# Kernel optimization log

Hardware: AMD Instinct MI355X
Metric: run time of the kernel (lower is better)

The kernel has to match this reference:

```python
import jax, jax.numpy as jnp
import numpy as np


def setup_inputs() -> dict:
    key = jax.random.key(0)
    ks = jax.random.split(key, 6)
    B, Lq, Lk, D = 8, 2048, 2048, 128
    return {
        "query": jax.random.normal(ks[0], (B, Lq, D), dtype=jnp.float32),
        "x": jax.random.normal(ks[1], (B, Lk, D), dtype=jnp.float32),
        "valid": jax.random.randint(ks[2], (B, Lq, Lk), 0, 2, dtype=jnp.int32),
        "Wq": jax.random.normal(ks[3], (D, D), dtype=jnp.float32) * 0.05,
        "Wk": jax.random.normal(ks[4], (D, D), dtype=jnp.float32) * 0.05,
        "Wv": jax.random.normal(ks[5], (D, D), dtype=jnp.float32) * 0.05,
    }


def reference(query, x, valid, Wq, Wk, Wv):
    # bias-free linear projections; torch Linear weight is [out, in] -> y = x @ W.T
    q = jnp.einsum("bqd,ad->bqa", query, Wq)   # [B, Lq, D]
    k = jnp.einsum("bkd,ad->bka", x, Wk)        # [B, Lk, D]
    v = jnp.einsum("bkd,ad->bka", x, Wv)        # [B, Lk, D]
    # scores (no scale arg passed in this config)
    att = jnp.einsum("bqd,bkd->bqk", q, k)      # [B, Lq, Lk]
    # max-subtraction BEFORE masking (matches original op order)
    att = att - jnp.max(att, axis=-1, keepdims=True)
    att = jnp.where(valid <= 0, -jnp.inf, att)
    att_w = jax.nn.softmax(att, axis=-1)
    # rows with all entries masked produce NaN -> fill with 0
    att_w = jnp.where(jnp.isnan(att_w), jnp.zeros_like(att_w), att_w)
    result = jnp.einsum("bqk,bkd->bqd", att_w, v)
    return (result, att_w)
```

## Files before the change

kernel.cpp:

```cpp
#include <hip/hip_runtime.h>
#include <float.h>
#include <math.h>


#define BB 8
#define LQ 2048
#define LK 2048
#define DD 128
#define NROWS (BB*LQ)
#define KS 4

typedef __attribute__((ext_vector_type(8))) _Float16 half8;
typedef __attribute__((ext_vector_type(4))) float f32x4;

#define QH_OFF  (0u)
#define QL_OFF  (1u*NROWS*DD*2u)
#define KH_OFF  (2u*NROWS*DD*2u)
#define KL_OFF  (3u*NROWS*DD*2u)
#define VTH_OFF (4u*NROWS*DD*2u)
#define VTL_OFF (5u*NROWS*DD*2u)
#define BM_OFF  (6u*NROWS*DD*2u)
#define MZ_OFF  (BM_OFF + (unsigned)NROWS*(LK/8))

__device__ __forceinline__ f32x4 mfma16(half8 a, half8 b, f32x4 c) {
  return __builtin_amdgcn_mfma_f32_16x16x32_f16(a, b, c, 0, 0, 0);
}

__global__ __launch_bounds__(256, 3) void proj_kernel(
    const float* __restrict__ query, const float* __restrict__ x,
    const float* __restrict__ Wq, const float* __restrict__ Wk,
    const float* __restrict__ Wv, unsigned char* __restrict__ wsb)
{
  __shared__ float SB[8704];
  const int which = blockIdx.y;
  const float* __restrict__ src = (which == 0) ? query : x;
  const float* __restrict__ W   = (which == 0) ? Wq : (which == 1 ? Wk : Wv);
  const int t = threadIdx.x, l = t & 63, wv = t >> 6;
  const int lr = l & 15, lg = l >> 4;
  const int r0 = blockIdx.x * 64;

#pragma unroll
  for (int j = 0; j < 8; ++j) {
    const int flat = j * 1024 + t * 4;
    const int row = flat >> 7, col = flat & 127;
    *(float4*)&SB[row * 132 + col] = *(const float4*)&src[(size_t)(r0 + row) * DD + col];
  }
  __syncthreads();

  half8 ah[4], al[4];
#pragma unroll
  for (int dc = 0; dc < 4; ++dc) {
    const int base = (wv * 16 + lr) * 132 + dc * 32 + lg * 8;
    float4 f0 = *(const float4*)&SB[base];
    float4 f1 = *(const float4*)&SB[base + 4];
    float f[8] = {f0.x, f0.y, f0.z, f0.w, f1.x, f1.y, f1.z, f1.w};
#pragma unroll
    for (int e = 0; e < 8; ++e) {
      _Float16 h = (_Float16)f[e];
      ah[dc][e] = h;
      al[dc][e] = (_Float16)(f[e] - (float)h);
    }
  }
  __syncthreads();

  f32x4 acc[8];
#pragma unroll
  for (int a = 0; a < 8; ++a) acc[a] = (f32x4){0.f, 0.f, 0.f, 0.f};

#pragma unroll
  for (int dc = 0; dc < 4; ++dc) {
#pragma unroll
    for (int a = 0; a < 8; ++a) {
      const float* p = W + (size_t)(a * 16 + lr) * DD + dc * 32 + lg * 8;
      float4 f0 = *(const float4*)p;
      float4 f1 = *(const float4*)(p + 4);
      float f[8] = {f0.x, f0.y, f0.z, f0.w, f1.x, f1.y, f1.z, f1.w};
      half8 bh, bl;
#pragma unroll
      for (int e = 0; e < 8; ++e) {
        _Float16 h = (_Float16)f[e];
        bh[e] = h;
        bl[e] = (_Float16)(f[e] - (float)h);
      }
      acc[a] = mfma16(ah[dc], bh, acc[a]);
      acc[a] = mfma16(al[dc], bh, acc[a]);
      acc[a] = mfma16(ah[dc], bl, acc[a]);
    }
  }

  if (which < 2) {
    _Float16* Oh = (_Float16*)(wsb + (which == 0 ? QH_OFF : KH_OFF));
    _Float16* Ol = (_Float16*)(wsb + (which == 0 ? QL_OFF : KL_OFF));
#pragma unroll
    for (int a = 0; a < 8; ++a)
#pragma unroll
      for (int i = 0; i < 4; ++i) {
        const int ro = r0 + wv * 16 + lg * 4 + i;
        const int co = a * 16 + lr;
        float v = acc[a][i];
        _Float16 h = (_Float16)v;
        Oh[(size_t)ro * DD + co] = h;
        Ol[(size_t)ro * DD + co] = (_Float16)(v - (float)h);
      }
  } else {
    _Float16* TH = (_Float16*)SB;
    _Float16* TL = TH + 8704;
#pragma unroll
    for (int a = 0; a < 8; ++a)
#pragma unroll
      for (int i = 0; i < 4; ++i) {
        const int rl = wv * 16 + lg * 4 + i;
        const int co = a * 16 + lr;
        float v = acc[a][i];
        _Float16 h = (_Float16)v;
        TH[co * 68 + rl] = h;
        TL[co * 68 + rl] = (_Float16)(v - (float)h);
      }
    __syncthreads();
    _Float16* Vh = (_Float16*)(wsb + VTH_OFF);
    _Float16* Vl = (_Float16*)(wsb + VTL_OFF);
    const int b = r0 >> 11, kloc = r0 & 2047;
    const int d = t >> 1, hh = t & 1;
    const size_t gb = ((size_t)(b * DD + d)) * LK + kloc + hh * 32;
#pragma unroll
    for (int j = 0; j < 8; ++j) {
      *(ushort4*)(Vh + gb + j * 4) = *(const ushort4*)&TH[d * 68 + hh * 32 + j * 4];
      *(ushort4*)(Vl + gb + j * 4) = *(const ushort4*)&TL[d * 68 + hh * 32 + j * 4];
    }
  }
}

__global__ __launch_bounds__(256) void maskpack_kernel(
    const int* __restrict__ valid, unsigned long long* __restrict__ bm)
{
  const int t = threadIdx.x, l = t & 63, wv = t >> 6;
  const size_t base = (size_t)blockIdx.x * 32768 + (size_t)wv * 8192;
  for (int it = 0; it < 32; ++it) {
    int v0 = valid[base + (size_t)(it * 4 + 0) * 64 + l];
    int v1 = valid[base + (size_t)(it * 4 + 1) * 64 + l];
    int v2 = valid[base + (size_t)(it * 4 + 2) * 64 + l];
    int v3 = valid[base + (size_t)(it * 4 + 3) * 64 + l];
    unsigned long long m0 = __ballot(v0 > 0);
    unsigned long long m1 = __ballot(v1 > 0);
    unsigned long long m2 = __ballot(v2 > 0);
    unsigned long long m3 = __ballot(v3 > 0);
    if (l == 0) {
      bm[(base >> 6) + it * 4 + 0] = m0;
      bm[(base >> 6) + it * 4 + 1] = m1;
      bm[(base >> 6) + it * 4 + 2] = m2;
      bm[(base >> 6) + it * 4 + 3] = m3;
    }
  }
}

__global__ __launch_bounds__(256, 4) void scores_kernel(
    const unsigned char* __restrict__ wsb, float* __restrict__ att)
{
  __shared__ _Float16 KHs[64 * 128];
  __shared__ _Float16 KLs[64 * 128];
  const int t = threadIdx.x, l = t & 63, wv = t >> 6;
  const int lr = l & 15, lg = l >> 4;
  const int qb = blockIdx.x, b = blockIdx.y, ks = blockIdx.z;
  const int rowg = b * LQ + qb * 64;
  const int kbase = ks * 512;
  const _Float16* QH = (const _Float16*)(wsb + QH_OFF);
  const _Float16* QL = (const _Float16*)(wsb + QL_OFF);
  const _Float16* KH = (const _Float16*)(wsb + KH_OFF);
  const _Float16* KL = (const _Float16*)(wsb + KL_OFF);
  const unsigned* bm32 = (const unsigned*)(wsb + BM_OFF);
  float* M = (float*)(wsb + MZ_OFF);
  float* Z = M + KS * NROWS;

  half8 qh[4], ql[4];
#pragma unroll
  for (int dc = 0; dc < 4; ++dc) {
    const size_t idx = ((size_t)(rowg + wv * 16 + lr)) * DD + dc * 32 + lg * 8;
    qh[dc] = *(const half8*)(QH + idx);
    ql[dc] = *(const half8*)(QL + idx);
  }

  half8 rh[4], rl[4];
  auto issue_stage = [&](int kt) {
#pragma unroll
    for (int j = 0; j < 4; ++j) {
      const int flat = j * 2048 + t * 8;
      const int row = flat >> 7, col = flat & 127;
      const size_t g = ((size_t)(b * LK + kbase + kt * 64 + row)) * DD + col;
      rh[j] = *(const half8*)(KH + g);
      rl[j] = *(const half8*)(KL + g);
    }
  };
  auto write_stage = [&]() {
#pragma unroll
    for (int j = 0; j < 4; ++j) {
      const int flat = j * 2048 + t * 8;
      const int row = flat >> 7, c8 = (flat >> 3) & 15;
      const int c8s = (c8 & 8) | ((c8 ^ row) & 7);
      *(half8*)&KHs[row * 128 + c8s * 8] = rh[j];
      *(half8*)&KLs[row * 128 + c8s * 8] = rl[j];
    }
  };

  issue_stage(0);
  write_stage();

  float m_run[4], z_run[4];
#pragma unroll
  for (int i = 0; i < 4; ++i) { m_run[i] = -FLT_MAX; z_run[i] = 0.f; }

  for (int kt = 0; kt < 8; ++kt) {
    const int k0 = kbase + kt * 64;
    if (kt < 7) issue_stage(kt + 1);
    unsigned mw0[4], mw1[4];
#pragma unroll
    for (int i = 0; i < 4; ++i) {
      uint2 u = *(const uint2*)(bm32 + ((size_t)(rowg + wv * 16 + lg * 4 + i)) * 64 + (k0 >> 5));
      mw0[i] = u.x; mw1[i] = u.y;
    }
    __syncthreads();

    f32x4 acc[4];
#pragma unroll
    for (int kg = 0; kg < 4; ++kg) acc[kg] = (f32x4){0.f, 0.f, 0.f, 0.f};
#pragma unroll
    for (int kg = 0; kg < 4; ++kg)
#pragma unroll
      for (int dc = 0; dc < 4; ++dc) {
        const int c8 = dc * 4 + lg;
        const int c8s = (c8 & 8) | ((c8 ^ lr) & 7);
        half8 bh = *(const half8*)&KHs[(kg * 16 + lr) * 128 + c8s * 8];
        half8 bl = *(const half8*)&KLs[(kg * 16 + lr) * 128 + c8s * 8];
        acc[kg] = mfma16(qh[dc], bh, acc[kg]);
        acc[kg] = mfma16(ql[dc], bh, acc[kg]);
        acc[kg] = mfma16(qh[dc], bl, acc[kg]);
      }

#pragma unroll
    for (int i = 0; i < 4; ++i) {
      float sv[4];
      float* ap = att + ((size_t)(rowg + wv * 16 + lg * 4 + i)) * LK + k0 + lr;
#pragma unroll
      for (int kg = 0; kg < 4; ++kg) {
        unsigned w = (kg < 2) ? mw0[i] : mw1[i];
        int bit = (w >> (((kg & 1) * 16) + lr)) & 1;
        float v = bit ? acc[kg][i] : -INFINITY;
        sv[kg] = v;
        ap[kg * 16] = v;
      }
      float tm = fmaxf(fmaxf(sv[0], sv[1]), fmaxf(sv[2], sv[3]));
#pragma unroll
      for (int o = 1; o < 16; o <<= 1) tm = fmaxf(tm, __shfl_xor(tm, o));
      const float mo = m_run[i], mn = fmaxf(mo, tm);
      float za = __expf(sv[0] - mn) + __expf(sv[1] - mn) +
                 __expf(sv[2] - mn) + __expf(sv[3] - mn);
      z_run[i] = z_run[i] * __expf(mo - mn) + za;
      m_run[i] = mn;
    }
    __syncthreads();
    if (kt < 7) write_stage();
  }

#pragma unroll
  for (int i = 0; i < 4; ++i) {
    float z = z_run[i];
#pragma unroll
    for (int o = 1; o < 16; o <<= 1) z += __shfl_xor(z, o);
    if (lr == 0) {
      const size_t row = (size_t)(rowg + wv * 16 + lg * 4 + i);
      M[(size_t)ks * NROWS + row] = m_run[i];
      Z[(size_t)ks * NROWS + row] = z;
    }
  }
}

__global__ __launch_bounds__(256, 4) void pv_kernel(
    const unsigned char* __restrict__ wsb, float* __restrict__ att,
    float* __restrict__ res)
{
  __shared__ _Float16 VHs[128 * 64];
  __shared__ _Float16 Wt[64 * 64];
  const int t = threadIdx.x, l = t & 63, wv = t >> 6;
  const int lr = l & 15, lg = l >> 4;
  const int qb = blockIdx.x, b = blockIdx.y, kp = blockIdx.z;
  const int rowg = b * LQ + qb * 64;
  const int kbase = kp * 512;
  const _Float16* VTH = (const _Float16*)(wsb + VTH_OFF);
  const float* M = (const float*)(wsb + MZ_OFF);
  const float* Z = M + KS * NROWS;

  const int srow = t >> 2, scb = (t & 3) * 16;
  float mg, zi;
  {
    const size_t row = (size_t)(rowg + srow);
    float m0 = M[row], m1 = M[NROWS + row], m2 = M[2 * NROWS + row], m3 = M[3 * NROWS + row];
    mg = fmaxf(fmaxf(m0, m1), fmaxf(m2, m3));
    float z = Z[row] * __expf(m0 - mg) + Z[NROWS + row] * __expf(m1 - mg) +
              Z[2 * NROWS + row] * __expf(m2 - mg) + Z[3 * NROWS + row] * __expf(m3 - mg);
    zi = (z > 0.f) ? 1.f / z : 0.f;
  }

  half8 vhr[4];
  float4 sr[4];
  auto issue_V = [&](int kt) {
#pragma unroll
    for (int j = 0; j < 4; ++j) {
      const int flat = j * 2048 + t * 8;
      const int d = flat >> 6, kk = flat & 63;
      vhr[j] = *(const half8*)(VTH + ((size_t)(b * DD + d)) * LK + kbase + kt * 64 + kk);
    }
  };
  auto issue_S = [&](int kt) {
    const size_t rb = (size_t)(rowg + srow) * LK + kbase + kt * 64 + scb;
#pragma unroll
    for (int j = 0; j < 4; ++j) sr[j] = *(const float4*)&att[rb + j * 4];
  };
  auto w_stage = [&](int kt) {
    const size_t rb = (size_t)(rowg + srow) * LK + kbase + kt * 64 + scb;
    float wf[16];
#pragma unroll
    for (int j = 0; j < 4; ++j) {
      float4 w4;
      w4.x = __expf(sr[j].x - mg) * zi;
      w4.y = __expf(sr[j].y - mg) * zi;
      w4.z = __expf(sr[j].z - mg) * zi;
      w4.w = __expf(sr[j].w - mg) * zi;
      *(float4*)&att[rb + j * 4] = w4;
      wf[j * 4 + 0] = w4.x; wf[j * 4 + 1] = w4.y;
      wf[j * 4 + 2] = w4.z; wf[j * 4 + 3] = w4.w;
    }
    half8 h0, h1;
#pragma unroll
    for (int e = 0; e < 8; ++e) { h0[e] = (_Float16)wf[e]; h1[e] = (_Float16)wf[8 + e]; }
    const int g0 = (t & 3) * 2;
    *(half8*)&Wt[srow * 64 + (((g0)     ^ srow) & 7) * 8] = h0;
    *(half8*)&Wt[srow * 64 + (((g0 + 1) ^ srow) & 7) * 8] = h1;
#pragma unroll
    for (int j = 0; j < 4; ++j) {
      const int flat = j * 2048 + t * 8;
      const int d = flat >> 6, c8 = (flat >> 3) & 7;
      *(half8*)&VHs[d * 64 + ((c8 ^ d) & 7) * 8] = vhr[j];
    }
  };

  f32x4 oacc[8];
#pragma unroll
  for (int df = 0; df < 8; ++df) oacc[df] = (f32x4){0.f, 0.f, 0.f, 0.f};

  issue_V(0); issue_S(0);
  w_stage(0);
  __syncthreads();

  for (int kt = 0; kt < 8; ++kt) {
    if (kt < 7) { issue_V(kt + 1); issue_S(kt + 1); }

#pragma unroll
    for (int kc = 0; kc < 2; ++kc) {
      const int c8 = kc * 4 + lg;
      half8 wfr = *(const half8*)&Wt[(wv * 16 + lr) * 64 + ((c8 ^ (lr & 7)) & 7) * 8];
#pragma unroll
      for (int df = 0; df < 8; ++df) {
        half8 vh = *(const half8*)&VHs[(df * 16 + lr) * 64 + ((c8 ^ (lr & 7)) & 7) * 8];
        oacc[df] = mfma16(wfr, vh, oacc[df]);
      }
    }
    __syncthreads();
    if (kt < 7) {
      w_stage(kt + 1);
      __syncthreads();
    }
  }

#pragma unroll
  for (int df = 0; df < 8; ++df)
#pragma unroll
    for (int i = 0; i < 4; ++i)
      atomicAdd(&res[((size_t)(rowg + wv * 16 + lg * 4 + i)) * DD + df * 16 + lr],
                oacc[df][i]);
}

extern "C" void kernel_launch(void* const* d_in, const int* in_sizes, int n_in,
                              void* d_out, int out_size, void* d_ws, size_t ws_size,
                              hipStream_t stream)
{
  (void)in_sizes; (void)n_in; (void)out_size; (void)ws_size;
  const float* query = (const float*)d_in[0];
  const float* x     = (const float*)d_in[1];
  const int*   valid = (const int*)d_in[2];
  const float* Wq    = (const float*)d_in[3];
  const float* Wk    = (const float*)d_in[4];
  const float* Wv    = (const float*)d_in[5];

  float* out = (float*)d_out;
  float* res = out;
  float* att = out + (size_t)NROWS * DD;
  unsigned char* wsb = (unsigned char*)d_ws;

  hipMemsetAsync(res, 0, (size_t)NROWS * DD * sizeof(float), stream);
  proj_kernel<<<dim3(NROWS / 64, 3), 256, 0, stream>>>(query, x, Wq, Wk, Wv, wsb);
  maskpack_kernel<<<dim3(1024), 256, 0, stream>>>(
      valid, (unsigned long long*)(wsb + BM_OFF));
  scores_kernel<<<dim3(LQ / 64, BB, KS), 256, 0, stream>>>(wsb, att);
  pv_kernel<<<dim3(LQ / 64, BB, KS), 256, 0, stream>>>(wsb, att, res);
}
```

Before: 416.7 us.

## Fuse scores and PV into one two-pass kernel, drop K/V low-precision splits

Replaces the separate scores and PV kernels with one fused kernel per 32-query block. The first pass computes row max and sum; the second recomputes QK^T, writes normalized weights directly and accumulates P·V in LDS. This removes the att write/read round trip, the split-K atomics and the memset. K and V are now stored only as single fp16 (no low-part correction), which cuts projection stores and MFMA work but lowers precision. Recomputing QK doubles the score MFMAs, and the grid is smaller (512 blocks), which may reduce occupancy.

After: 365.5 us. -12.3%, faster.

```diff
diff --git a/kernel.cpp b/kernel.cpp
--- a/kernel.cpp
+++ b/kernel.cpp
@@ -8,19 +8,16 @@
 #define LK 2048
 #define DD 128
 #define NROWS (BB*LQ)
-#define KS 4
+#define QB 32
 
 typedef __attribute__((ext_vector_type(8))) _Float16 half8;
 typedef __attribute__((ext_vector_type(4))) float f32x4;
 
 #define QH_OFF  (0u)
-#define QL_OFF  (1u*NROWS*DD*2u)
-#define KH_OFF  (2u*NROWS*DD*2u)
-#define KL_OFF  (3u*NROWS*DD*2u)
-#define VTH_OFF (4u*NROWS*DD*2u)
-#define VTL_OFF (5u*NROWS*DD*2u)
-#define BM_OFF  (6u*NROWS*DD*2u)
-#define MZ_OFF  (BM_OFF + (unsigned)NROWS*(LK/8))
+#define QL_OFF  (4194304u)
+#define KH_OFF  (8388608u)
+#define VTH_OFF (12582912u)
+#define BM_OFF  (16777216u)
 
 __device__ __forceinline__ f32x4 mfma16(half8 a, half8 b, f32x4 c) {
   return __builtin_amdgcn_mfma_f32_16x16x32_f16(a, b, c, 0, 0, 0);
@@ -88,9 +85,9 @@
     }
   }
 
-  if (which < 2) {
-    _Float16* Oh = (_Float16*)(wsb + (which == 0 ? QH_OFF : KH_OFF));
-    _Float16* Ol = (_Float16*)(wsb + (which == 0 ? QL_OFF : KL_OFF));
+  if (which == 0) {
+    _Float16* Oh = (_Float16*)(wsb + QH_OFF);
+    _Float16* Ol = (_Float16*)(wsb + QL_OFF);
 #pragma unroll
     for (int a = 0; a < 8; ++a)
 #pragma unroll
@@ -102,31 +99,34 @@
         Oh[(size_t)ro * DD + co] = h;
         Ol[(size_t)ro * DD + co] = (_Float16)(v - (float)h);
       }
+  } else if (which == 1) {
+    _Float16* Oh = (_Float16*)(wsb + KH_OFF);
+#pragma unroll
+    for (int a = 0; a < 8; ++a)
+#pragma unroll
+      for (int i = 0; i < 4; ++i) {
+        const int ro = r0 + wv * 16 + lg * 4 + i;
+        const int co = a * 16 + lr;
+        Oh[(size_t)ro * DD + co] = (_Float16)acc[a][i];
+      }
   } else {
     _Float16* TH = (_Float16*)SB;
-    _Float16* TL = TH + 8704;
 #pragma unroll
     for (int a = 0; a < 8; ++a)
 #pragma unroll
       for (int i = 0; i < 4; ++i) {
         const int rl = wv * 16 + lg * 4 + i;
         const int co = a * 16 + lr;
-        float v = acc[a][i];
-        _Float16 h = (_Float16)v;
-        TH[co * 68 + rl] = h;
-        TL[co * 68 + rl] = (_Float16)(v - (float)h);
+        TH[co * 68 + rl] = (_Float16)acc[a][i];
       }
     __syncthreads();
     _Float16* Vh = (_Float16*)(wsb + VTH_OFF);
-    _Float16* Vl = (_Float16*)(wsb + VTL_OFF);
     const int b = r0 >> 11, kloc = r0 & 2047;
     const int d = t >> 1, hh = t & 1;
     const size_t gb = ((size_t)(b * DD + d)) * LK + kloc + hh * 32;
 #pragma unroll
-    for (int j = 0; j < 8; ++j) {
+    for (int j = 0; j < 8; ++j)
       *(ushort4*)(Vh + gb + j * 4) = *(const ushort4*)&TH[d * 68 + hh * 32 + j * 4];
-      *(ushort4*)(Vl + gb + j * 4) = *(const ushort4*)&TL[d * 68 + hh * 32 + j * 4];
-    }
   }
 }
 
@@ -153,111 +153,114 @@
   }
 }
 
-__global__ __launch_bounds__(256, 4) void scores_kernel(
-    const unsigned char* __restrict__ wsb, float* __restrict__ att)
+__global__ __launch_bounds__(256, 2) void fused_kernel(
+    const unsigned char* __restrict__ wsb,
+    float* __restrict__ att, float* __restrict__ res)
 {
-  __shared__ _Float16 KHs[64 * 128];
-  __shared__ _Float16 KLs[64 * 128];
+  __shared__ __align__(16) unsigned char SM[37376];
+  _Float16* KHs = (_Float16*)SM;
+  _Float16* Vs  = (_Float16*)(SM + 16384);
+  _Float16* Wt  = (_Float16*)(SM + 32768);
+  float*    MZ  = (float*)(SM + 36864);
+  float*    Osum = (float*)SM;
+
   const int t = threadIdx.x, l = t & 63, wv = t >> 6;
   const int lr = l & 15, lg = l >> 4;
-  const int qb = blockIdx.x, b = blockIdx.y, ks = blockIdx.z;
-  const int rowg = b * LQ + qb * 64;
-  const int kbase = ks * 512;
+  const int rg = wv >> 1, kh = wv & 1;
+  const int lin = blockIdx.x;
+  const int b = lin & 7, qb = lin >> 3;
+  const int rowg = b * LQ + qb * QB;
+
   const _Float16* QH = (const _Float16*)(wsb + QH_OFF);
   const _Float16* QL = (const _Float16*)(wsb + QL_OFF);
   const _Float16* KH = (const _Float16*)(wsb + KH_OFF);
-  const _Float16* KL = (const _Float16*)(wsb + KL_OFF);
+  const _Float16* VT = (const _Float16*)(wsb + VTH_OFF);
   const unsigned* bm32 = (const unsigned*)(wsb + BM_OFF);
-  float* M = (float*)(wsb + MZ_OFF);
-  float* Z = M + KS * NROWS;
 
   half8 qh[4], ql[4];
 #pragma unroll
   for (int dc = 0; dc < 4; ++dc) {
-    const size_t idx = ((size_t)(rowg + wv * 16 + lr)) * DD + dc * 32 + lg * 8;
+    const size_t idx = ((size_t)(rowg + rg * 16 + lr)) * DD + dc * 32 + lg * 8;
     qh[dc] = *(const half8*)(QH + idx);
     ql[dc] = *(const half8*)(QL + idx);
   }
 
-  half8 rh[4], rl[4];
-  auto issue_stage = [&](int kt) {
+  half8 rk[4], rv[4];
+  auto issueK = [&](int kt) {
 #pragma unroll
     for (int j = 0; j < 4; ++j) {
       const int flat = j * 2048 + t * 8;
       const int row = flat >> 7, col = flat & 127;
-      const size_t g = ((size_t)(b * LK + kbase + kt * 64 + row)) * DD + col;
-      rh[j] = *(const half8*)(KH + g);
-      rl[j] = *(const half8*)(KL + g);
-    }
-  };
-  auto write_stage = [&]() {
+      rk[j] = *(const half8*)(KH + ((size_t)(b * LK + kt * 64 + row)) * DD + col);
+    }
+  };
+  auto writeK = [&]() {
 #pragma unroll
     for (int j = 0; j < 4; ++j) {
       const int flat = j * 2048 + t * 8;
       const int row = flat >> 7, c8 = (flat >> 3) & 15;
       const int c8s = (c8 & 8) | ((c8 ^ row) & 7);
-      *(half8*)&KHs[row * 128 + c8s * 8] = rh[j];
-      *(half8*)&KLs[row * 128 + c8s * 8] = rl[j];
-    }
-  };
-
-  issue_stage(0);
-  write_stage();
-
-  float m_run[4], z_run[4];
-#pragma unroll
-  for (int i = 0; i < 4; ++i) { m_run[i] = -FLT_MAX; z_run[i] = 0.f; }
-
-  for (int kt = 0; kt < 8; ++kt) {
-    const int k0 = kbase + kt * 64;
-    if (kt < 7) issue_stage(kt + 1);
-    unsigned mw0[4], mw1[4];
-#pragma unroll
-    for (int i = 0; i < 4; ++i) {
-      uint2 u = *(const uint2*)(bm32 + ((size_t)(rowg + wv * 16 + lg * 4 + i)) * 64 + (k0 >> 5));
-      mw0[i] = u.x; mw1[i] = u.y;
-    }
-    __syncthreads();
-
-    f32x4 acc[4];
-#pragma unroll
-    for (int kg = 0; kg < 4; ++kg) acc[kg] = (f32x4){0.f, 0.f, 0.f, 0.f};
-#pragma unroll
-    for (int kg = 0; kg < 4; ++kg)
+      *(half8*)&KHs[row * 128 + c8s * 8] = rk[j];
+    }
+  };
+  auto issueV = [&](int kt) {
+#pragma unroll
+    for (int j = 0; j < 4; ++j) {
+      const int flat = j * 2048 + t * 8;
+      const int d = flat >> 6, kk = flat & 63;
+      rv[j] = *(const half8*)(VT + ((size_t)(b * DD + d)) * LK + kt * 64 + kk);
+    }
+  };
+  auto writeV = [&]() {
+#pragma unroll
+    for (int j = 0; j < 4; ++j) {
+      const int flat = j * 2048 + t * 8;
+      const int d = flat >> 6, c8 = (flat >> 3) & 7;
+      *(half8*)&Vs[d * 64 + ((c8 ^ d) & 7) * 8] = rv[j];
+    }
+  };
+  auto computeQK = [&](f32x4* acc) {
+    acc[0] = (f32x4){0.f, 0.f, 0.f, 0.f};
+    acc[1] = (f32x4){0.f, 0.f, 0.f, 0.f};
+#pragma unroll
+    for (int g = 0; g < 2; ++g)
 #pragma unroll
       for (int dc = 0; dc < 4; ++dc) {
         const int c8 = dc * 4 + lg;
         const int c8s = (c8 & 8) | ((c8 ^ lr) & 7);
-        half8 bh = *(const half8*)&KHs[(kg * 16 + lr) * 128 + c8s * 8];
-        half8 bl = *(const half8*)&KLs[(kg * 16 + lr) * 128 + c8s * 8];
-        acc[kg] = mfma16(qh[dc], bh, acc[kg]);
-        acc[kg] = mfma16(ql[dc], bh, acc[kg]);
-        acc[kg] = mfma16(qh[dc], bl, acc[kg]);
-      }
-
+        half8 bh = *(const half8*)&KHs[((2 * kh + g) * 16 + lr) * 128 + c8s * 8];
+        acc[g] = mfma16(ql[dc], bh, acc[g]);
+        acc[g] = mfma16(qh[dc], bh, acc[g]);
+      }
+  };
+
+  float m_run[4], z_run[4];
+#pragma unroll
+  for (int i = 0; i < 4; ++i) { m_run[i] = -FLT_MAX; z_run[i] = 0.f; }
+
+  issueK(0); writeK();
+  for (int kt = 0; kt < 32; ++kt) {
+    if (kt < 31) issueK(kt + 1);
+    unsigned mw[4];
+#pragma unroll
+    for (int i = 0; i < 4; ++i)
+      mw[i] = bm32[((size_t)(rowg + rg * 16 + lg * 4 + i)) * 64 + kt * 2 + kh];
+    __syncthreads();
+    f32x4 acc[2];
+    computeQK(acc);
 #pragma unroll
     for (int i = 0; i < 4; ++i) {
-      float sv[4];
-      float* ap = att + ((size_t)(rowg + wv * 16 + lg * 4 + i)) * LK + k0 + lr;
-#pragma unroll
-      for (int kg = 0; kg < 4; ++kg) {
-        unsigned w = (kg < 2) ? mw0[i] : mw1[i];
-        int bit = (w >> (((kg & 1) * 16) + lr)) & 1;
-        float v = bit ? acc[kg][i] : -INFINITY;
-        sv[kg] = v;
-        ap[kg * 16] = v;
-      }
-      float tm = fmaxf(fmaxf(sv[0], sv[1]), fmaxf(sv[2], sv[3]));
+      float sv0 = ((mw[i] >> lr) & 1) ? acc[0][i] : -INFINITY;
+      float sv1 = ((mw[i] >> (16 + lr)) & 1) ? acc[1][i] : -INFINITY;
+      float tm = fmaxf(sv0, sv1);
 #pragma unroll
       for (int o = 1; o < 16; o <<= 1) tm = fmaxf(tm, __shfl_xor(tm, o));
       const float mo = m_run[i], mn = fmaxf(mo, tm);
-      float za = __expf(sv[0] - mn) + __expf(sv[1] - mn) +
-                 __expf(sv[2] - mn) + __expf(sv[3] - mn);
-      z_run[i] = z_run[i] * __expf(mo - mn) + za;
+      z_run[i] = z_run[i] * __expf(mo - mn) + __expf(sv0 - mn) + __expf(sv1 - mn);
       m_run[i] = mn;
     }
     __syncthreads();
-    if (kt < 7) write_stage();
+    if (kt < 31) writeK();
   }
 
 #pragma unroll
@@ -266,116 +269,90 @@
 #pragma unroll
     for (int o = 1; o < 16; o <<= 1) z += __shfl_xor(z, o);
     if (lr == 0) {
-      const size_t row = (size_t)(rowg + wv * 16 + lg * 4 + i);
-      M[(size_t)ks * NROWS + row] = m_run[i];
-      Z[(size_t)ks * NROWS + row] = z;
-    }
-  }
-}
-
-__global__ __launch_bounds__(256, 4) void pv_kernel(
-    const unsigned char* __restrict__ wsb, float* __restrict__ att,
-    float* __restrict__ res)
-{
-  __shared__ _Float16 VHs[128 * 64];
-  __shared__ _Float16 Wt[64 * 64];
-  const int t = threadIdx.x, l = t & 63, wv = t >> 6;
-  const int lr = l & 15, lg = l >> 4;
-  const int qb = blockIdx.x, b = blockIdx.y, kp = blockIdx.z;
-  const int rowg = b * LQ + qb * 64;
-  const int kbase = kp * 512;
-  const _Float16* VTH = (const _Float16*)(wsb + VTH_OFF);
-  const float* M = (const float*)(wsb + MZ_OFF);
-  const float* Z = M + KS * NROWS;
-
-  const int srow = t >> 2, scb = (t & 3) * 16;
-  float mg, zi;
-  {
-    const size_t row = (size_t)(rowg + srow);
-    float m0 = M[row], m1 = M[NROWS + row], m2 = M[2 * NROWS + row], m3 = M[3 * NROWS + row];
-    mg = fmaxf(fmaxf(m0, m1), fmaxf(m2, m3));
-    float z = Z[row] * __expf(m0 - mg) + Z[NROWS + row] * __expf(m1 - mg) +
-              Z[2 * NROWS + row] * __expf(m2 - mg) + Z[3 * NROWS + row] * __expf(m3 - mg);
-    zi = (z > 0.f) ? 1.f / z : 0.f;
-  }
-
-  half8 vhr[4];
-  float4 sr[4];
-  auto issue_V = [&](int kt) {
-#pragma unroll
-    for (int j = 0; j < 4; ++j) {
-      const int flat = j * 2048 + t * 8;
-      const int d = flat >> 6, kk = flat & 63;
-      vhr[j] = *(const half8*)(VTH + ((size_t)(b * DD + d)) * LK + kbase + kt * 64 + kk);
-    }
-  };
-  auto issue_S = [&](int kt) {
-    const size_t rb = (size_t)(rowg + srow) * LK + kbase + kt * 64 + scb;
-#pragma unroll
-    for (int j = 0; j < 4; ++j) sr[j] = *(const float4*)&att[rb + j * 4];
-  };
-  auto w_stage = [&](int kt) {
-    const size_t rb = (size_t)(rowg + srow) * LK + kbase + kt * 64 + scb;
-    float wf[16];
-#pragma unroll
-    for (int j = 0; j < 4; ++j) {
-      float4 w4;
-      w4.x = __expf(sr[j].x - mg) * zi;
-      w4.y = __expf(sr[j].y - mg) * zi;
-      w4.z = __expf(sr[j].z - mg) * zi;
-      w4.w = __expf(sr[j].w - mg) * zi;
-      *(float4*)&att[rb + j * 4] = w4;
-      wf[j * 4 + 0] = w4.x; wf[j * 4 + 1] = w4.y;
-      wf[j * 4 + 2] = w4.z; wf[j * 4 + 3] = w4.w;
-    }
-    half8 h0, h1;
-#pragma unroll
-    for (int e = 0; e < 8; ++e) { h0[e] = (_Float16)wf[e]; h1[e] = (_Float16)wf[8 + e]; }
-    const int g0 = (t & 3) * 2;
-    *(half8*)&Wt[srow * 64 + (((g0)     ^ srow) & 7) * 8] = h0;
-    *(half8*)&Wt[srow * 64 + (((g0 + 1) ^ srow) & 7) * 8] = h1;
-#pragma unroll
-    for (int j = 0; j < 4; ++j) {
-      const int flat = j * 2048 + t * 8;
-      const int d = flat >> 6, c8 = (flat >> 3) & 7;
-      *(half8*)&VHs[d * 64 + ((c8 ^ d) & 7) * 8] = vhr[j];
-    }
-  };
+      MZ[(wv * 16 + lg * 4 + i) * 2]     = m_run[i];
+      MZ[(wv * 16 + lg * 4 + i) * 2 + 1] = z;
+    }
+  }
+  __syncthreads();
+  float mf[4], zif[4];
+#pragma unroll
+  for (int i = 0; i < 4; ++i) {
+    const int r = lg * 4 + i, pw = wv ^ 1;
+    float m1 = MZ[(wv * 16 + r) * 2], z1 = MZ[(wv * 16 + r) * 2 + 1];
+    float m2 = MZ[(pw * 16 + r) * 2], z2 = MZ[(pw * 16 + r) * 2 + 1];
+    float m = fmaxf(m1, m2);
+    float z = z1 * __expf(m1 - m) + z2 * __expf(m2 - m);
+    mf[i] = m;
+    zif[i] = (z > 0.f) ? 1.f / z : 0.f;
+  }
 
   f32x4 oacc[8];
 #pragma unroll
   for (int df = 0; df < 8; ++df) oacc[df] = (f32x4){0.f, 0.f, 0.f, 0.f};
 
-  issue_V(0); issue_S(0);
-  w_stage(0);
-  __syncthreads();
-
-  for (int kt = 0; kt < 8; ++kt) {
-    if (kt < 7) { issue_V(kt + 1); issue_S(kt + 1); }
-
-#pragma unroll
-    for (int kc = 0; kc < 2; ++kc) {
-      const int c8 = kc * 4 + lg;
-      half8 wfr = *(const half8*)&Wt[(wv * 16 + lr) * 64 + ((c8 ^ (lr & 7)) & 7) * 8];
+  issueK(0); issueV(0);
+  writeK(); writeV();
+  for (int kt = 0; kt < 32; ++kt) {
+    if (kt < 31) { issueK(kt + 1); issueV(kt + 1); }
+    unsigned mw[4];
+#pragma unroll
+    for (int i = 0; i < 4; ++i)
+      mw[i] = bm32[((size_t)(rowg + rg * 16 + lg * 4 + i)) * 64 + kt * 2 + kh];
+    __syncthreads();
+    f32x4 acc[2];
+    computeQK(acc);
+#pragma unroll
+    for (int i = 0; i < 4; ++i) {
+      const int rloc = rg * 16 + lg * 4 + i;
+      float* ap = att + ((size_t)(rowg + rloc)) * LK + kt * 64 + kh * 32 + lr;
+#pragma unroll
+      for (int g = 0; g < 2; ++g) {
+        const int bit = (mw[i] >> (g * 16 + lr)) & 1;
+        float sm_ = bit ? acc[g][i] : -INFINITY;
+        float w = __expf(sm_ - mf[i]) * zif[i];
+        ap[g * 16] = w;
+        const int c = kh * 32 + g * 16 + lr;
+        Wt[rloc * 64 + (((c >> 3) ^ (rloc & 7)) & 7) * 8 + (c & 7)] = (_Float16)w;
+      }
+    }
+    asm volatile("" ::: "memory");
+    {
+      const int c8s = ((kh * 4 + lg) ^ (lr & 7)) & 7;
+      half8 pa = *(const half8*)&Wt[(rg * 16 + lr) * 64 + c8s * 8];
 #pragma unroll
       for (int df = 0; df < 8; ++df) {
-        half8 vh = *(const half8*)&VHs[(df * 16 + lr) * 64 + ((c8 ^ (lr & 7)) & 7) * 8];
-        oacc[df] = mfma16(wfr, vh, oacc[df]);
-      }
-    }
-    __syncthreads();
-    if (kt < 7) {
-      w_stage(kt + 1);
-      __syncthreads();
-    }
-  }
-
-#pragma unroll
-  for (int df = 0; df < 8; ++df)
-#pragma unroll
-    for (int i = 0; i < 4; ++i)
-      atomicAdd(&res[((size_t)(rowg + wv * 16 + lg * 4 + i)) * DD + df * 16 + lr],
-                oacc[df][i]);
+        half8 vb = *(const half8*)&Vs[(df * 16 + lr) * 64 + c8s * 8];
+        oacc[df] = mfma16(pa, vb, oacc[df]);
+      }
+    }
+    __syncthreads();
+    if (kt < 31) { writeK(); writeV(); }
+  }
+
+  if (kh == 1) {
+#pragma unroll
+    for (int df = 0; df < 8; ++df)
+#pragma unroll
+      for (int i = 0; i < 4; ++i)
+        Osum[(rg * 16 + lg * 4 + i) * 132 + df * 16 + lr] = oacc[df][i];
+  }
+  __syncthreads();
+  if (kh == 0) {
+#pragma unroll
+    for (int df = 0; df < 8; ++df)
+#pragma unroll
+      for (int i = 0; i < 4; ++i) {
+        const int idx = (rg * 16 + lg * 4 + i) * 132 + df * 16 + lr;
+        Osum[idx] += oacc[df][i];
+      }
+  }
+  __syncthreads();
+#pragma unroll
+  for (int j = 0; j < 4; ++j) {
+    const int flat = j * 1024 + t * 4;
+    const int r = flat >> 7, d = flat & 127;
+    *(float4*)&res[((size_t)(rowg + r)) * DD + d] = *(const float4*)&Osum[r * 132 + d];
+  }
 }
 
 extern "C" void kernel_launch(void* const* d_in, const int* in_sizes, int n_in,
@@ -395,10 +372,8 @@
   float* att = out + (size_t)NROWS * DD;
   unsigned char* wsb = (unsigned char*)d_ws;
 
-  hipMemsetAsync(res, 0, (size_t)NROWS * DD * sizeof(float), stream);
   proj_kernel<<<dim3(NROWS / 64, 3), 256, 0, stream>>>(query, x, Wq, Wk, Wv, wsb);
   maskpack_kernel<<<dim3(1024), 256, 0, stream>>>(
       valid, (unsigned long long*)(wsb + BM_OFF));
-  scores_kernel<<<dim3(LQ / 64, BB, KS), 256, 0, stream>>>(wsb, att);
-  pv_kernel<<<dim3(LQ / 64, BB, KS), 256, 0, stream>>>(wsb, att, res);
-}
+  fused_kernel<<<dim3(512), 256, 0, stream>>>(wsb, att, res);
+}
```
